# Kernel tuning notes

Hardware: AMD Instinct MI355X
Metric: run time of the kernel (lower is better)

The kernel has to match this reference:

```python
import jax, jax.numpy as jnp
import numpy as np

D = 512
H_G = 8
H_L = 8
WIN = 2
B = 4
S = 2048
LN_EPS = 1e-5


def layer_norm(x, g, b):
    m = jnp.mean(x, axis=-1, keepdims=True)
    v = jnp.mean(jnp.square(x - m), axis=-1, keepdims=True)
    return (x - m) * jax.lax.rsqrt(v + LN_EPS) * g + b


def mha(x, w_in, b_in, w_out, b_out, n_heads, mask=None):
    # x: [B', S', D]; w_in: [3D, D]; torch nn.MultiheadAttention math (eval, no dropout)
    Bp, Sp, Dm = x.shape
    dh = Dm // n_heads
    qkv = x @ w_in.T + b_in                      # [B', S', 3D]
    q, k, v = jnp.split(qkv, 3, axis=-1)
    sp = lambda t: t.reshape(Bp, Sp, n_heads, dh).transpose(0, 2, 1, 3)
    q, k, v = sp(q), sp(k), sp(v)                # [B', H, S', dh]
    scale = 1.0 / np.sqrt(dh).astype(np.float32)
    scores = jnp.einsum('bhqd,bhkd->bhqk', q, k) * scale
    if mask is not None:
        scores = scores + mask
    attn = jax.nn.softmax(scores, axis=-1)
    out = jnp.einsum('bhqk,bhkd->bhqd', attn, v)
    out = out.transpose(0, 2, 1, 3).reshape(Bp, Sp, Dm)
    return out @ w_out.T + b_out


def setup_inputs() -> dict:
    key = jax.random.key(0)
    ks = jax.random.split(key, 12)
    s = 0.02
    inp = {
        'x': jax.random.normal(ks[0], (B, S, D), jnp.float32),
        'ln1_g': jnp.ones((D,), jnp.float32), 'ln1_b': jnp.zeros((D,), jnp.float32),
        'ln2_g': jnp.ones((D,), jnp.float32), 'ln2_b': jnp.zeros((D,), jnp.float32),
        'ln3_g': jnp.ones((D,), jnp.float32), 'ln3_b': jnp.zeros((D,), jnp.float32),
        'gw_in': jax.random.normal(ks[1], (3 * D, D), jnp.float32) * s,
        'gb_in': jnp.zeros((3 * D,), jnp.float32),
        'gw_out': jax.random.normal(ks[2], (D, D), jnp.float32) * s,
        'gb_out': jnp.zeros((D,), jnp.float32),
        'lw_in': jax.random.normal(ks[3], (3 * D, D), jnp.float32) * s,
        'lb_in': jnp.zeros((3 * D,), jnp.float32),
        'lw_out': jax.random.normal(ks[4], (D, D), jnp.float32) * s,
        'lb_out': jnp.zeros((D,), jnp.float32),
        'gate_w': jax.random.normal(ks[5], (D, D), jnp.float32) * s,
        'gate_b': jnp.zeros((D,), jnp.float32),
        'ff_w1': jax.random.normal(ks[6], (4 * D, D), jnp.float32) * s,
        'ff_b1': jnp.zeros((4 * D,), jnp.float32),
        'ff_w2': jax.random.normal(ks[7], (D, 4 * D), jnp.float32) * s,
        'ff_b2': jnp.zeros((D,), jnp.float32),
    }
    return inp


def reference(x, ln1_g, ln1_b, ln2_g, ln2_b, ln3_g, ln3_b,
              gw_in, gb_in, gw_out, gb_out,
              lw_in, lb_in, lw_out, lb_out,
              gate_w, gate_b, ff_w1, ff_b1, ff_w2, ff_b2):
    Bb, Ss, Dm = x.shape
    x_norm = layer_norm(x, ln1_g, ln1_b)

    # global causal attention
    causal = jnp.triu(jnp.full((Ss, Ss), -jnp.inf, jnp.float32), 1)
    g_out = mha(x_norm, gw_in, gb_in, gw_out, gb_out, H_G, mask=causal)

    xl = x_norm.reshape(Bb * (Ss // WIN), WIN, Dm)
    l_out = mha(xl, lw_in, lb_in, lw_out, lb_out, H_L).reshape(Bb, Ss, Dm)

    gate = jax.nn.sigmoid(x_norm @ gate_w.T + gate_b)
    x = x + gate * g_out + (1.0 - gate) * l_out

    h = layer_norm(x, ln2_g, ln2_b)
    h = jax.nn.gelu(h @ ff_w1.T + ff_b1, approximate=False) @ ff_w2.T + ff_b2
    x = x + h
    return layer_norm(x, ln3_g, ln3_b)
```

## Files before the change

### kernel.cpp

```cpp
#include <hip/hip_runtime.h>
#include <math.h>
#include <stdint.h>

typedef unsigned short u16;
typedef __attribute__((ext_vector_type(4))) unsigned short u16x4;
typedef __attribute__((ext_vector_type(8))) unsigned short u16x8;
typedef __attribute__((ext_vector_type(8))) short s16x8;
typedef __attribute__((ext_vector_type(4))) float f32x4;

constexpr int Bc = 4;
constexpr int Sq = 2048;
constexpr int Dm = 512;
constexpr int Mrows = Bc * Sq;

__device__ inline float b2f(u16 h) {
  union { uint32_t u; float f; } x; x.u = (uint32_t)h << 16; return x.f;
}
__device__ inline u16 f2bf(float f) {
  union { float f; uint32_t u; } x; x.f = f;
  uint32_t r = (x.u + 0x7fffu + ((x.u >> 16) & 1u)) >> 16;
  return (u16)r;
}

constexpr size_t W_GWIN  = 0;
constexpr size_t W_LWIN  = 786432;
constexpr size_t W_GWOUT = 1572864;
constexpr size_t W_LWOUT = 1835008;
constexpr size_t W_GATE  = 2097152;
constexpr size_t W_FF1   = 2359296;
constexpr size_t W_FF2   = 3407872;
constexpr size_t W_TOTAL = 4456448;

__global__ __launch_bounds__(256) void wconv_kernel(
    const float* __restrict__ gw_in, const float* __restrict__ lw_in,
    const float* __restrict__ gw_out, const float* __restrict__ lw_out,
    const float* __restrict__ gate_w, const float* __restrict__ ff_w1,
    const float* __restrict__ ff_w2, u16* __restrict__ dst) {
  size_t idx = ((size_t)blockIdx.x * 256 + threadIdx.x) * 4;
  if (idx >= W_TOTAL) return;
  const float* src; size_t base;
  if      (idx < W_LWIN)  { src = gw_in;  base = W_GWIN;  }
  else if (idx < W_GWOUT) { src = lw_in;  base = W_LWIN;  }
  else if (idx < W_LWOUT) { src = gw_out; base = W_GWOUT; }
  else if (idx < W_GATE)  { src = lw_out; base = W_LWOUT; }
  else if (idx < W_FF1)   { src = gate_w; base = W_GATE;  }
  else if (idx < W_FF2)   { src = ff_w1;  base = W_FF1;   }
  else                    { src = ff_w2;  base = W_FF2;   }
  float4 v = *reinterpret_cast<const float4*>(src + (idx - base));
  u16x4 o = { f2bf(v.x), f2bf(v.y), f2bf(v.z), f2bf(v.w) };
  *reinterpret_cast<u16x4*>(dst + idx) = o;
}

template <bool OB>
__global__ __launch_bounds__(128) void ln_kernel(
    const float* __restrict__ in, const float* __restrict__ add,
    const float* __restrict__ g, const float* __restrict__ b,
    void* __restrict__ outp) {
  const int row = blockIdx.x;
  const int t = threadIdx.x;
  float4 v = reinterpret_cast<const float4*>(in + (size_t)row * Dm)[t];
  if (add != nullptr) {
    float4 a = reinterpret_cast<const float4*>(add + (size_t)row * Dm)[t];
    v.x += a.x; v.y += a.y; v.z += a.z; v.w += a.w;
  }
  float s  = v.x + v.y + v.z + v.w;
  float s2 = v.x*v.x + v.y*v.y + v.z*v.z + v.w*v.w;
  #pragma unroll
  for (int o = 32; o > 0; o >>= 1) {
    s  += __shfl_down(s, o);
    s2 += __shfl_down(s2, o);
  }
  __shared__ float rs[2], rs2[2];
  if ((t & 63) == 0) { rs[t >> 6] = s; rs2[t >> 6] = s2; }
  __syncthreads();
  const float mean = (rs[0] + rs[1]) * (1.0f / Dm);
  const float var  = (rs2[0] + rs2[1]) * (1.0f / Dm) - mean * mean;
  const float rstd = rsqrtf(var + 1e-5f);
  float4 gv = reinterpret_cast<const float4*>(g)[t];
  float4 bv = reinterpret_cast<const float4*>(b)[t];
  float ox = (v.x - mean) * rstd * gv.x + bv.x;
  float oy = (v.y - mean) * rstd * gv.y + bv.y;
  float oz = (v.z - mean) * rstd * gv.z + bv.z;
  float ow = (v.w - mean) * rstd * gv.w + bv.w;
  if (OB) {
    u16x4 o4 = { f2bf(ox), f2bf(oy), f2bf(oz), f2bf(ow) };
    *reinterpret_cast<u16x4*>((u16*)outp + (size_t)row * Dm + t * 4) = o4;
  } else {
    float4 o4; o4.x = ox; o4.y = oy; o4.z = oz; o4.w = ow;
    reinterpret_cast<float4*>((float*)outp + (size_t)row * Dm)[t] = o4;
  }
}

template <int ACT, bool OUT_BF16>
__global__ __launch_bounds__(256) void mfma_gemm(
    const u16* __restrict__ A, const u16* __restrict__ W,
    const float* __restrict__ bias, void* __restrict__ Cout, int N, int K) {
  __shared__ u16 sA[128 * 32];
  __shared__ u16 sW[128 * 32];
  const int tid  = threadIdx.x;
  const int wid  = tid >> 6, lane = tid & 63;
  const int lr   = lane & 15, kh = lane >> 4;
  const int wm   = wid >> 1, wn = wid & 1;
  const int m0   = blockIdx.y * 128, n0 = blockIdx.x * 128;
  const int row0 = tid >> 2,        ko0 = (tid & 3) * 8;
  const int row1 = (256 + tid) >> 2, ko1 = (tid & 3) * 8;

  f32x4 acc[4][4] = {};
  for (int k0 = 0; k0 < K; k0 += 32) {
    __syncthreads();
    __builtin_amdgcn_global_load_lds(
        (const __attribute__((address_space(1))) void*)(A + (size_t)(m0 + row0) * K + k0 + ko0),
        (__attribute__((address_space(3))) void*)(sA + wid * 512), 16, 0, 0);
    __builtin_amdgcn_global_load_lds(
        (const __attribute__((address_space(1))) void*)(A + (size_t)(m0 + row1) * K + k0 + ko1),
        (__attribute__((address_space(3))) void*)(sA + 2048 + wid * 512), 16, 0, 0);
    __builtin_amdgcn_global_load_lds(
        (const __attribute__((address_space(1))) void*)(W + (size_t)(n0 + row0) * K + k0 + ko0),
        (__attribute__((address_space(3))) void*)(sW + wid * 512), 16, 0, 0);
    __builtin_amdgcn_global_load_lds(
        (const __attribute__((address_space(1))) void*)(W + (size_t)(n0 + row1) * K + k0 + ko1),
        (__attribute__((address_space(3))) void*)(sW + 2048 + wid * 512), 16, 0, 0);
    __syncthreads();
    s16x8 af[4], bf[4];
    #pragma unroll
    for (int mf = 0; mf < 4; ++mf)
      af[mf] = *reinterpret_cast<const s16x8*>(&sA[(wm * 64 + mf * 16 + lr) * 32 + kh * 8]);
    #pragma unroll
    for (int nf = 0; nf < 4; ++nf)
      bf[nf] = *reinterpret_cast<const s16x8*>(&sW[(wn * 64 + nf * 16 + lr) * 32 + kh * 8]);
    #pragma unroll
    for (int mf = 0; mf < 4; ++mf)
      #pragma unroll
      for (int nf = 0; nf < 4; ++nf)
        acc[mf][nf] = __builtin_amdgcn_mfma_f32_16x16x32_bf16(af[mf], bf[nf], acc[mf][nf], 0, 0, 0);
  }
  #pragma unroll
  for (int nf = 0; nf < 4; ++nf) {
    const int col = n0 + wn * 64 + nf * 16 + lr;
    const float bv = bias[col];
    #pragma unroll
    for (int mf = 0; mf < 4; ++mf) {
      #pragma unroll
      for (int j = 0; j < 4; ++j) {
        const int rowg = m0 + wm * 64 + mf * 16 + kh * 4 + j;
        float v = acc[mf][nf][j] + bv;
        if (ACT == 1) v = 1.0f / (1.0f + expf(-v));
        else if (ACT == 2) v = 0.5f * v * (1.0f + erff(v * 0.70710678118654752440f));
        if (OUT_BF16) ((u16*)Cout)[(size_t)rowg * N + col] = f2bf(v);
        else          ((float*)Cout)[(size_t)rowg * N + col] = v;
      }
    }
  }
}

__global__ __launch_bounds__(256) void fuse3_kernel(
    const u16* __restrict__ A0, const u16* __restrict__ A1, const u16* __restrict__ A2,
    const u16* __restrict__ Wg, const u16* __restrict__ Wgo, const u16* __restrict__ Wlo,
    const float* __restrict__ bg, const float* __restrict__ bgo, const float* __restrict__ blo,
    const float* __restrict__ x, float* __restrict__ x2) {
  constexpr int N = 512, K = 512;
  __shared__ u16 sA[128 * 32];
  __shared__ u16 sW[128 * 32];
  const int tid  = threadIdx.x;
  const int wid  = tid >> 6, lane = tid & 63;
  const int lr   = lane & 15, kh = lane >> 4;
  const int wm   = wid >> 1, wn = wid & 1;
  const int m0   = blockIdx.y * 128, n0 = blockIdx.x * 128;
  const int row0 = tid >> 2,        ko0 = (tid & 3) * 8;
  const int row1 = (256 + tid) >> 2, ko1 = (tid & 3) * 8;

  f32x4 gv[4][4], pgv[4][4], acc[4][4];
  for (int pass = 0; pass < 3; ++pass) {
    const u16* A = (pass == 0) ? A0 : (pass == 1) ? A1 : A2;
    const u16* W = (pass == 0) ? Wg : (pass == 1) ? Wgo : Wlo;
    #pragma unroll
    for (int mf = 0; mf < 4; ++mf)
      #pragma unroll
      for (int nf = 0; nf < 4; ++nf)
        acc[mf][nf] = f32x4{0.f, 0.f, 0.f, 0.f};
    for (int k0 = 0; k0 < K; k0 += 32) {
      __syncthreads();
      __builtin_amdgcn_global_load_lds(
          (const __attribute__((address_space(1))) void*)(A + (size_t)(m0 + row0) * K + k0 + ko0),
          (__attribute__((address_space(3))) void*)(sA + wid * 512), 16, 0, 0);
      __builtin_amdgcn_global_load_lds(
          (const __attribute__((address_space(1))) void*)(A + (size_t)(m0 + row1) * K + k0 + ko1),
          (__attribute__((address_space(3))) void*)(sA + 2048 + wid * 512), 16, 0, 0);
      __builtin_amdgcn_global_load_lds(
          (const __attribute__((address_space(1))) void*)(W + (size_t)(n0 + row0) * K + k0 + ko0),
          (__attribute__((address_space(3))) void*)(sW + wid * 512), 16, 0, 0);
      __builtin_amdgcn_global_load_lds(
          (const __attribute__((address_space(1))) void*)(W + (size_t)(n0 + row1) * K + k0 + ko1),
          (__attribute__((address_space(3))) void*)(sW + 2048 + wid * 512), 16, 0, 0);
      __syncthreads();
      s16x8 af[4], bf[4];
      #pragma unroll
      for (int mf = 0; mf < 4; ++mf)
        af[mf] = *reinterpret_cast<const s16x8*>(&sA[(wm * 64 + mf * 16 + lr) * 32 + kh * 8]);
      #pragma unroll
      for (int nf = 0; nf < 4; ++nf)
        bf[nf] = *reinterpret_cast<const s16x8*>(&sW[(wn * 64 + nf * 16 + lr) * 32 + kh * 8]);
      #pragma unroll
      for (int mf = 0; mf < 4; ++mf)
        #pragma unroll
        for (int nf = 0; nf < 4; ++nf)
          acc[mf][nf] = __builtin_amdgcn_mfma_f32_16x16x32_bf16(af[mf], bf[nf], acc[mf][nf], 0, 0, 0);
    }
    if (pass == 0) {
      #pragma unroll
      for (int nf = 0; nf < 4; ++nf) {
        const float bv = bg[n0 + wn * 64 + nf * 16 + lr];
        #pragma unroll
        for (int mf = 0; mf < 4; ++mf)
          #pragma unroll
          for (int j = 0; j < 4; ++j)
            gv[mf][nf][j] = 1.0f / (1.0f + __expf(-(acc[mf][nf][j] + bv)));
      }
    } else if (pass == 1) {
      #pragma unroll
      for (int nf = 0; nf < 4; ++nf) {
        const float bv = bgo[n0 + wn * 64 + nf * 16 + lr];
        #pragma unroll
        for (int mf = 0; mf < 4; ++mf)
          #pragma unroll
          for (int j = 0; j < 4; ++j)
            pgv[mf][nf][j] = acc[mf][nf][j] + bv;
      }
    }
  }
  #pragma unroll
  for (int nf = 0; nf < 4; ++nf) {
    const int col = n0 + wn * 64 + nf * 16 + lr;
    const float bv = blo[col];
    #pragma unroll
    for (int mf = 0; mf < 4; ++mf) {
      #pragma unroll
      for (int j = 0; j < 4; ++j) {
        const int rowg = m0 + wm * 64 + mf * 16 + kh * 4 + j;
        const float pl = acc[mf][nf][j] + bv;
        const float g  = gv[mf][nf][j];
        const float pg = pgv[mf][nf][j];
        x2[(size_t)rowg * N + col] = x[(size_t)rowg * N + col] + g * pg + (1.0f - g) * pl;
      }
    }
  }
}

__global__ __launch_bounds__(256) void attn_global_kernel(
    const u16* __restrict__ qkv, u16* __restrict__ outb,
    float* __restrict__ opart, float* __restrict__ ml) {
  const int id = 79 - (int)blockIdx.x;
  int qt, s, ns;
  if (id < 8)       { qt = id;                s = 0;            ns = 1; }
  else if (id < 24) { int t = id - 8;  qt = 8 + (t >> 1);  s = t & 1;  ns = 2; }
  else if (id < 48) { int t = id - 24; int q3 = t / 3; qt = 16 + q3; s = t - q3 * 3; ns = 3; }
  else              { int t = id - 48; qt = 24 + (t >> 2); s = t & 3;  ns = 4; }
  const int kt0 = s * 8;
  const int kt1 = min(kt0 + 8, qt + 1);

  const int h  = blockIdx.y;
  const int b  = blockIdx.z;
  const int tid = threadIdx.x;
  const int w = tid >> 6, lane = tid & 63;
  const int c = lane & 15, kh = lane >> 4;

  __shared__ u16 Kb[64][72];
  __shared__ u16 Vt[64][72];
  __shared__ u16 Pw[4][16][72];

  const size_t bbase = (size_t)b * Sq;

  s16x8 aq[2];
  {
    const u16* qg = qkv + (bbase + qt * 64 + w * 16 + c) * 1536 + h * 64 + kh * 8;
    aq[0] = *reinterpret_cast<const s16x8*>(qg);
    aq[1] = *reinterpret_cast<const s16x8*>(qg + 32);
  }

  f32x4 o_acc[4] = {};
  float mrow[4] = { -INFINITY, -INFINITY, -INFINITY, -INFINITY };
  float lrow[4] = { 0.f, 0.f, 0.f, 0.f };
  int qp[4];
  #pragma unroll
  for (int j = 0; j < 4; ++j) qp[j] = qt * 64 + w * 16 + kh * 4 + j;

  const int g2 = tid >> 3, cc = tid & 7;
  const int srow2 = g2 * 2;
  const u16* kg0 = qkv + (bbase + srow2) * 1536 + 512 + h * 64 + cc * 8;
  const size_t tilestep = (size_t)64 * 1536;

  u16x8 ka, kb2, va, vb;
  {
    const u16* p = kg0 + (size_t)kt0 * tilestep;
    ka  = *reinterpret_cast<const u16x8*>(p);
    kb2 = *reinterpret_cast<const u16x8*>(p + 1536);
    va  = *reinterpret_cast<const u16x8*>(p + 512);
    vb  = *reinterpret_cast<const u16x8*>(p + 1536 + 512);
  }

  for (int kt = kt0; kt < kt1; ++kt) {
    __syncthreads();
    {
      *reinterpret_cast<u16x8*>(&Kb[srow2][cc * 8])     = ka;
      *reinterpret_cast<u16x8*>(&Kb[srow2 + 1][cc * 8]) = kb2;
      const int sw = srow2 ^ (cc * 8);
      #pragma unroll
      for (int i = 0; i < 8; ++i) {
        uint32_t pk = (uint32_t)va[i] | ((uint32_t)vb[i] << 16);
        *reinterpret_cast<uint32_t*>(&Vt[cc * 8 + i][sw]) = pk;
      }
    }
    __syncthreads();
    if (kt + 1 < kt1) {
      const u16* p = kg0 + (size_t)(kt + 1) * tilestep;
      ka  = *reinterpret_cast<const u16x8*>(p);
      kb2 = *reinterpret_cast<const u16x8*>(p + 1536);
      va  = *reinterpret_cast<const u16x8*>(p + 512);
      vb  = *reinterpret_cast<const u16x8*>(p + 1536 + 512);
    }

    f32x4 s_acc[4] = {};
    #pragma unroll
    for (int nb = 0; nb < 4; ++nb) {
      #pragma unroll
      for (int kk = 0; kk < 2; ++kk) {
        s16x8 bk = *reinterpret_cast<const s16x8*>(&Kb[nb * 16 + c][kk * 32 + kh * 8]);
        s_acc[nb] = __builtin_amdgcn_mfma_f32_16x16x32_bf16(aq[kk], bk, s_acc[nb], 0, 0, 0);
      }
    }

    const bool diag = (kt == qt);
    float p[4][4];
    float tm[4] = { -INFINITY, -INFINITY, -INFINITY, -INFINITY };
    #pragma unroll
    for (int nb = 0; nb < 4; ++nb) {
      #pragma unroll
      for (int j = 0; j < 4; ++j) {
        float sv = s_acc[nb][j] * 0.125f;
        if (diag && (kt * 64 + nb * 16 + c) > qp[j]) sv = -INFINITY;
        p[nb][j] = sv;
        tm[j] = fmaxf(tm[j], sv);
      }
    }
    #pragma unroll
    for (int o = 1; o < 16; o <<= 1) {
      #pragma unroll
      for (int j = 0; j < 4; ++j) tm[j] = fmaxf(tm[j], __shfl_xor(tm[j], o));
    }
    float corr[4], psum[4];
    #pragma unroll
    for (int j = 0; j < 4; ++j) {
      const float mnew = fmaxf(mrow[j], tm[j]);
      corr[j] = __expf(mrow[j] - mnew);
      mrow[j] = mnew;
      psum[j] = 0.f;
      #pragma unroll
      for (int nb = 0; nb < 4; ++nb) {
        p[nb][j] = __expf(p[nb][j] - mnew);
        psum[j] += p[nb][j];
      }
    }
    #pragma unroll
    for (int o = 1; o < 16; o <<= 1) {
      #pragma unroll
      for (int j = 0; j < 4; ++j) psum[j] += __shfl_xor(psum[j], o);
    }
    #pragma unroll
    for (int j = 0; j < 4; ++j) lrow[j] = lrow[j] * corr[j] + psum[j];
    #pragma unroll
    for (int nb2 = 0; nb2 < 4; ++nb2)
      #pragma unroll
      for (int j = 0; j < 4; ++j) o_acc[nb2][j] *= corr[j];

    #pragma unroll
    for (int nb = 0; nb < 4; ++nb)
      #pragma unroll
      for (int j = 0; j < 4; ++j)
        Pw[w][kh * 4 + j][nb * 16 + c] = f2bf(p[nb][j]);

    #pragma unroll
    for (int kk = 0; kk < 2; ++kk) {
      s16x8 ap = *reinterpret_cast<const s16x8*>(&Pw[w][c][kk * 32 + kh * 8]);
      #pragma unroll
      for (int nb2 = 0; nb2 < 4; ++nb2) {
        const int dh = nb2 * 16 + c;
        const int f8 = ((dh >> 3) & 7) * 8;
        s16x8 bv = *reinterpret_cast<const s16x8*>(&Vt[dh][(kk * 32 + kh * 8) ^ f8]);
        o_acc[nb2] = __builtin_amdgcn_mfma_f32_16x16x32_bf16(ap, bv, o_acc[nb2], 0, 0, 0);
      }
    }
  }

  if (ns == 1) {
    float invl[4];
    #pragma unroll
    for (int j = 0; j < 4; ++j) invl[j] = 1.0f / lrow[j];
    #pragma unroll
    for (int nb2 = 0; nb2 < 4; ++nb2)
      #pragma unroll
      for (int j = 0; j < 4; ++j) {
        const int qrow = qt * 64 + w * 16 + kh * 4 + j;
        outb[(bbase + qrow) * Dm + h * 64 + nb2 * 16 + c] = f2bf(o_acc[nb2][j] * invl[j]);
      }
  } else {
    const size_t pid = (size_t)(b * 8 + h) * 80 + id;
    float* op = opart + pid * 4096;
    #pragma unroll
    for (int nb2 = 0; nb2 < 4; ++nb2)
      #pragma unroll
      for (int j = 0; j < 4; ++j)
        op[(w * 16 + kh * 4 + j) * 64 + nb2 * 16 + c] = o_acc[nb2][j];
    if (c == 0) {
      #pragma unroll
      for (int j = 0; j < 4; ++j) {
        ml[pid * 128 + w * 16 + kh * 4 + j]      = mrow[j];
        ml[pid * 128 + 64 + w * 16 + kh * 4 + j] = lrow[j];
      }
    }
  }
}

__global__ __launch_bounds__(256) void attn_combine_kernel(
    const float* __restrict__ opart, const float* __restrict__ ml,
    u16* __restrict__ outb) {
  const int qt = 8 + (int)blockIdx.x;
  const int h = blockIdx.y, b = blockIdx.z;
  int ns, idb;
  if (qt < 16)      { ns = 2; idb = 8 + (qt - 8) * 2; }
  else if (qt < 24) { ns = 3; idb = 24 + (qt - 16) * 3; }
  else              { ns = 4; idb = 48 + (qt - 24) * 4; }
  const int r  = threadIdx.x >> 2;
  const int d0 = (threadIdx.x & 3) * 16;
  const size_t pidb = (size_t)(b * 8 + h) * 80 + idb;

  float M = -INFINITY;
  for (int s2 = 0; s2 < ns; ++s2)
    M = fmaxf(M, ml[(pidb + s2) * 128 + r]);
  float L = 0.f;
  f32x4 o0 = {}, o1 = {}, o2 = {}, o3 = {};
  for (int s2 = 0; s2 < ns; ++s2) {
    const size_t pp = pidb + s2;
    const float wgt = __expf(ml[pp * 128 + r] - M);
    L += wgt * ml[pp * 128 + 64 + r];
    const float* op = opart + pp * 4096 + (size_t)r * 64 + d0;
    f32x4 a0 = *reinterpret_cast<const f32x4*>(op);
    f32x4 a1 = *reinterpret_cast<const f32x4*>(op + 4);
    f32x4 a2 = *reinterpret_cast<const f32x4*>(op + 8);
    f32x4 a3 = *reinterpret_cast<const f32x4*>(op + 12);
    #pragma unroll
    for (int i = 0; i < 4; ++i) {
      o0[i] += wgt * a0[i]; o1[i] += wgt * a1[i];
      o2[i] += wgt * a2[i]; o3[i] += wgt * a3[i];
    }
  }
  const float invL = 1.0f / L;
  u16* dst = outb + ((size_t)b * Sq + qt * 64 + r) * Dm + h * 64 + d0;
  u16x4 w0 = { f2bf(o0[0]*invL), f2bf(o0[1]*invL), f2bf(o0[2]*invL), f2bf(o0[3]*invL) };
  u16x4 w1 = { f2bf(o1[0]*invL), f2bf(o1[1]*invL), f2bf(o1[2]*invL), f2bf(o1[3]*invL) };
  u16x4 w2 = { f2bf(o2[0]*invL), f2bf(o2[1]*invL), f2bf(o2[2]*invL), f2bf(o2[3]*invL) };
  u16x4 w3 = { f2bf(o3[0]*invL), f2bf(o3[1]*invL), f2bf(o3[2]*invL), f2bf(o3[3]*invL) };
  *reinterpret_cast<u16x4*>(dst)      = w0;
  *reinterpret_cast<u16x4*>(dst + 4)  = w1;
  *reinterpret_cast<u16x4*>(dst + 8)  = w2;
  *reinterpret_cast<u16x4*>(dst + 12) = w3;
}

__global__ __launch_bounds__(256) void attn_local_kernel(
    const u16* __restrict__ qkv, u16* __restrict__ outb) {
  const int unit = blockIdx.x * 4 + (threadIdx.x >> 6);
  const int lane = threadIdx.x & 63;
  const int h = unit & 7;
  const size_t pair = (size_t)(unit >> 3);
  const u16* r0 = qkv + pair * 2 * 1536;
  const u16* r1 = r0 + 1536;
  const int off = h * 64 + lane;
  const float q0 = b2f(r0[off]), k0 = b2f(r0[512 + off]), v0 = b2f(r0[1024 + off]);
  const float q1 = b2f(r1[off]), k1 = b2f(r1[512 + off]), v1 = b2f(r1[1024 + off]);
  float s00 = q0 * k0, s01 = q0 * k1, s10 = q1 * k0, s11 = q1 * k1;
  #pragma unroll
  for (int o = 1; o < 64; o <<= 1) {
    s00 += __shfl_xor(s00, o); s01 += __shfl_xor(s01, o);
    s10 += __shfl_xor(s10, o); s11 += __shfl_xor(s11, o);
  }
  s00 *= 0.125f; s01 *= 0.125f; s10 *= 0.125f; s11 *= 0.125f;
  const float m0 = fmaxf(s00, s01), m1 = fmaxf(s10, s11);
  const float e00 = expf(s00 - m0), e01 = expf(s01 - m0);
  const float e10 = expf(s10 - m1), e11 = expf(s11 - m1);
  const float w0 = 1.0f / (e00 + e01), w1 = 1.0f / (e10 + e11);
  outb[pair * 2 * Dm + off]       = f2bf((e00 * v0 + e01 * v1) * w0);
  outb[(pair * 2 + 1) * Dm + off] = f2bf((e10 * v0 + e11 * v1) * w1);
}

extern "C" void kernel_launch(void* const* d_in, const int* in_sizes, int n_in,
                              void* d_out, int out_size, void* d_ws, size_t ws_size,
                              hipStream_t stream) {
  const float* x      = (const float*)d_in[0];
  const float* ln1_g  = (const float*)d_in[1];
  const float* ln1_b  = (const float*)d_in[2];
  const float* ln2_g  = (const float*)d_in[3];
  const float* ln2_b  = (const float*)d_in[4];
  const float* ln3_g  = (const float*)d_in[5];
  const float* ln3_b  = (const float*)d_in[6];
  const float* gw_in  = (const float*)d_in[7];
  const float* gb_in  = (const float*)d_in[8];
  const float* gw_out = (const float*)d_in[9];
  const float* gb_out = (const float*)d_in[10];
  const float* lw_in  = (const float*)d_in[11];
  const float* lb_in  = (const float*)d_in[12];
  const float* lw_out = (const float*)d_in[13];
  const float* lb_out = (const float*)d_in[14];
  const float* gate_w = (const float*)d_in[15];
  const float* gate_b = (const float*)d_in[16];
  const float* ff_w1  = (const float*)d_in[17];
  const float* ff_b1  = (const float*)d_in[18];
  const float* ff_w2  = (const float*)d_in[19];
  const float* ff_b2  = (const float*)d_in[20];
  float* out = (float*)d_out;
  char* wsb  = (char*)d_ws;

  float* opart = (float*)(wsb + 0);
  float* ml    = (float*)(wsb + 41943040);
  float* x2    = (float*)(wsb + 0);
  float* h2    = (float*)(wsb + 16777216);
  u16*   xnb   = (u16*)(wsb + 67108864);
  u16*   qkvb  = (u16*)(wsb + 75497472);
  u16*   attgb = (u16*)(wsb + 100663296);
  u16*   attlb = (u16*)(wsb + 109051904);
  u16*   wb    = (u16*)(wsb + 117440512);
  u16*   ff1b  = qkvb;

  wconv_kernel<<<(W_TOTAL / 4 + 255) / 256, 256, 0, stream>>>(
      gw_in, lw_in, gw_out, lw_out, gate_w, ff_w1, ff_w2, wb);
  ln_kernel<true><<<Mrows, 128, 0, stream>>>(x, nullptr, ln1_g, ln1_b, xnb);
  mfma_gemm<0, true><<<dim3(1536 / 128, Mrows / 128), 256, 0, stream>>>(
      xnb, wb + W_LWIN, lb_in, qkvb, 1536, 512);
  attn_local_kernel<<<(Mrows / 2) * 8 / 4, 256, 0, stream>>>(qkvb, attlb);
  mfma_gemm<0, true><<<dim3(1536 / 128, Mrows / 128), 256, 0, stream>>>(
      xnb, wb + W_GWIN, gb_in, qkvb, 1536, 512);
  attn_global_kernel<<<dim3(80, 8, Bc), 256, 0, stream>>>(qkvb, attgb, opart, ml);
  attn_combine_kernel<<<dim3(24, 8, Bc), 256, 0, stream>>>(opart, ml, attgb);
  fuse3_kernel<<<dim3(512 / 128, Mrows / 128), 256, 0, stream>>>(
      xnb, attgb, attlb, wb + W_GATE, wb + W_GWOUT, wb + W_LWOUT,
      gate_b, gb_out, lb_out, x, x2);
  ln_kernel<true><<<Mrows, 128, 0, stream>>>(x2, nullptr, ln2_g, ln2_b, xnb);
  mfma_gemm<2, true><<<dim3(2048 / 128, Mrows / 128), 256, 0, stream>>>(
      xnb, wb + W_FF1, ff_b1, ff1b, 2048, 512);
  mfma_gemm<0, false><<<dim3(512 / 128, Mrows / 128), 256, 0, stream>>>(
      ff1b, wb + W_FF2, ff_b2, h2, 512, 2048);
  ln_kernel<false><<<Mrows, 128, 0, stream>>>(x2, h2, ln3_g, ln3_b, out);
}
```

Measured before the change: 298.4 us.

## Merge QKV GEMMs, split-K the FF2 GEMM, use exp2 softmax in attention

The global and local QKV projections become a single GEMM of width 3072, which relies on the global and local in_proj weights sitting next to each other in the bf16 weight buffer; a second bias pointer is selected by column. The FF2 GEMM (K=2048, only 256 tiles) is split-K into two halves that write separate fp32 buffers, and the final layernorm sums both. Global attention now works in the exp2 domain with a prescaled log2e factor and defers the row-sum shuffle reduction to after the key loop, and the partial buffer indexing is compacted to 72 slots. The aim is fewer launches, better GPU occupancy for the FF2 GEMM, and less per-tile shuffle work, at the cost of an extra fp32 partial buffer read and write.

```diff
diff --git a/kernel.cpp b/kernel.cpp
--- a/kernel.cpp
+++ b/kernel.cpp
@@ -12,6 +12,7 @@
 constexpr int Sq = 2048;
 constexpr int Dm = 512;
 constexpr int Mrows = Bc * Sq;
+constexpr int QW = 3072;
 
 __device__ inline float b2f(u16 h) {
   union { uint32_t u; float f; } x; x.u = (uint32_t)h << 16; return x.f;
@@ -54,6 +55,7 @@
 template <bool OB>
 __global__ __launch_bounds__(128) void ln_kernel(
     const float* __restrict__ in, const float* __restrict__ add,
+    const float* __restrict__ add2,
     const float* __restrict__ g, const float* __restrict__ b,
     void* __restrict__ outp) {
   const int row = blockIdx.x;
@@ -61,6 +63,10 @@
   float4 v = reinterpret_cast<const float4*>(in + (size_t)row * Dm)[t];
   if (add != nullptr) {
     float4 a = reinterpret_cast<const float4*>(add + (size_t)row * Dm)[t];
+    v.x += a.x; v.y += a.y; v.z += a.z; v.w += a.w;
+  }
+  if (add2 != nullptr) {
+    float4 a = reinterpret_cast<const float4*>(add2 + (size_t)row * Dm)[t];
     v.x += a.x; v.y += a.y; v.z += a.z; v.w += a.w;
   }
   float s  = v.x + v.y + v.z + v.w;
@@ -94,7 +100,8 @@
 template <int ACT, bool OUT_BF16>
 __global__ __launch_bounds__(256) void mfma_gemm(
     const u16* __restrict__ A, const u16* __restrict__ W,
-    const float* __restrict__ bias, void* __restrict__ Cout, int N, int K) {
+    const float* __restrict__ bias, const float* __restrict__ bias2, int bsplit,
+    void* __restrict__ Cout, int N, int K) {
   __shared__ u16 sA[128 * 32];
   __shared__ u16 sW[128 * 32];
   const int tid  = threadIdx.x;
@@ -137,7 +144,7 @@
   #pragma unroll
   for (int nf = 0; nf < 4; ++nf) {
     const int col = n0 + wn * 64 + nf * 16 + lr;
-    const float bv = bias[col];
+    const float bv = (bias2 != nullptr && col >= bsplit) ? bias2[col - bsplit] : bias[col];
     #pragma unroll
     for (int mf = 0; mf < 4; ++mf) {
       #pragma unroll
@@ -148,6 +155,67 @@
         else if (ACT == 2) v = 0.5f * v * (1.0f + erff(v * 0.70710678118654752440f));
         if (OUT_BF16) ((u16*)Cout)[(size_t)rowg * N + col] = f2bf(v);
         else          ((float*)Cout)[(size_t)rowg * N + col] = v;
+      }
+    }
+  }
+}
+
+__global__ __launch_bounds__(256) void mfma_gemm_sk(
+    const u16* __restrict__ A, const u16* __restrict__ W,
+    const float* __restrict__ bias, float* __restrict__ C0, float* __restrict__ C1,
+    int N, int Kt) {
+  __shared__ u16 sA[128 * 32];
+  __shared__ u16 sW[128 * 32];
+  const int tid  = threadIdx.x;
+  const int wid  = tid >> 6, lane = tid & 63;
+  const int lr   = lane & 15, kh = lane >> 4;
+  const int wm   = wid >> 1, wn = wid & 1;
+  const int m0   = blockIdx.y * 128, n0 = blockIdx.x * 128;
+  const int z    = blockIdx.z;
+  const int kbeg = z * (Kt / 2), kend = kbeg + (Kt / 2);
+  const int row0 = tid >> 2,        ko0 = (tid & 3) * 8;
+  const int row1 = (256 + tid) >> 2, ko1 = (tid & 3) * 8;
+
+  f32x4 acc[4][4] = {};
+  for (int k0 = kbeg; k0 < kend; k0 += 32) {
+    __syncthreads();
+    __builtin_amdgcn_global_load_lds(
+        (const __attribute__((address_space(1))) void*)(A + (size_t)(m0 + row0) * Kt + k0 + ko0),
+        (__attribute__((address_space(3))) void*)(sA + wid * 512), 16, 0, 0);
+    __builtin_amdgcn_global_load_lds(
+        (const __attribute__((address_space(1))) void*)(A + (size_t)(m0 + row1) * Kt + k0 + ko1),
+        (__attribute__((address_space(3))) void*)(sA + 2048 + wid * 512), 16, 0, 0);
+    __builtin_amdgcn_global_load_lds(
+        (const __attribute__((address_space(1))) void*)(W + (size_t)(n0 + row0) * Kt + k0 + ko0),
+        (__attribute__((address_space(3))) void*)(sW + wid * 512), 16, 0, 0);
+    __builtin_amdgcn_global_load_lds(
+        (const __attribute__((address_space(1))) void*)(W + (size_t)(n0 + row1) * Kt + k0 + ko1),
+        (__attribute__((address_space(3))) void*)(sW + 2048 + wid * 512), 16, 0, 0);
+    __syncthreads();
+    s16x8 af[4], bf[4];
+    #pragma unroll
+    for (int mf = 0; mf < 4; ++mf)
+      af[mf] = *reinterpret_cast<const s16x8*>(&sA[(wm * 64 + mf * 16 + lr) * 32 + kh * 8]);
+    #pragma unroll
+    for (int nf = 0; nf < 4; ++nf)
+      bf[nf] = *reinterpret_cast<const s16x8*>(&sW[(wn * 64 + nf * 16 + lr) * 32 + kh * 8]);
+    #pragma unroll
+    for (int mf = 0; mf < 4; ++mf)
+      #pragma unroll
+      for (int nf = 0; nf < 4; ++nf)
+        acc[mf][nf] = __builtin_amdgcn_mfma_f32_16x16x32_bf16(af[mf], bf[nf], acc[mf][nf], 0, 0, 0);
+  }
+  float* C = z ? C1 : C0;
+  #pragma unroll
+  for (int nf = 0; nf < 4; ++nf) {
+    const int col = n0 + wn * 64 + nf * 16 + lr;
+    const float bv = z ? 0.0f : bias[col];
+    #pragma unroll
+    for (int mf = 0; mf < 4; ++mf) {
+      #pragma unroll
+      for (int j = 0; j < 4; ++j) {
+        const int rowg = m0 + wm * 64 + mf * 16 + kh * 4 + j;
+        C[(size_t)rowg * N + col] = acc[mf][nf][j] + bv;
       }
     }
   }
@@ -263,6 +331,7 @@
   const int tid = threadIdx.x;
   const int w = tid >> 6, lane = tid & 63;
   const int c = lane & 15, kh = lane >> 4;
+  constexpr float TS = 0.125f * 1.44269504088896f;
 
   __shared__ u16 Kb[64][72];
   __shared__ u16 Vt[64][72];
@@ -272,7 +341,7 @@
 
   s16x8 aq[2];
   {
-    const u16* qg = qkv + (bbase + qt * 64 + w * 16 + c) * 1536 + h * 64 + kh * 8;
+    const u16* qg = qkv + (bbase + qt * 64 + w * 16 + c) * QW + h * 64 + kh * 8;
     aq[0] = *reinterpret_cast<const s16x8*>(qg);
     aq[1] = *reinterpret_cast<const s16x8*>(qg + 32);
   }
@@ -286,16 +355,16 @@
 
   const int g2 = tid >> 3, cc = tid & 7;
   const int srow2 = g2 * 2;
-  const u16* kg0 = qkv + (bbase + srow2) * 1536 + 512 + h * 64 + cc * 8;
-  const size_t tilestep = (size_t)64 * 1536;
+  const u16* kg0 = qkv + (bbase + srow2) * QW + 512 + h * 64 + cc * 8;
+  const size_t tilestep = (size_t)64 * QW;
 
   u16x8 ka, kb2, va, vb;
   {
     const u16* p = kg0 + (size_t)kt0 * tilestep;
     ka  = *reinterpret_cast<const u16x8*>(p);
-    kb2 = *reinterpret_cast<const u16x8*>(p + 1536);
+    kb2 = *reinterpret_cast<const u16x8*>(p + QW);
     va  = *reinterpret_cast<const u16x8*>(p + 512);
-    vb  = *reinterpret_cast<const u16x8*>(p + 1536 + 512);
+    vb  = *reinterpret_cast<const u16x8*>(p + QW + 512);
   }
 
   for (int kt = kt0; kt < kt1; ++kt) {
@@ -314,9 +383,9 @@
     if (kt + 1 < kt1) {
       const u16* p = kg0 + (size_t)(kt + 1) * tilestep;
       ka  = *reinterpret_cast<const u16x8*>(p);
-      kb2 = *reinterpret_cast<const u16x8*>(p + 1536);
+      kb2 = *reinterpret_cast<const u16x8*>(p + QW);
       va  = *reinterpret_cast<const u16x8*>(p + 512);
-      vb  = *reinterpret_cast<const u16x8*>(p + 1536 + 512);
+      vb  = *reinterpret_cast<const u16x8*>(p + QW + 512);
     }
 
     f32x4 s_acc[4] = {};
@@ -336,7 +405,7 @@
     for (int nb = 0; nb < 4; ++nb) {
       #pragma unroll
       for (int j = 0; j < 4; ++j) {
-        float sv = s_acc[nb][j] * 0.125f;
+        float sv = s_acc[nb][j] * TS;
         if (diag && (kt * 64 + nb * 16 + c) > qp[j]) sv = -INFINITY;
         p[nb][j] = sv;
         tm[j] = fmaxf(tm[j], sv);
@@ -347,30 +416,21 @@
       #pragma unroll
       for (int j = 0; j < 4; ++j) tm[j] = fmaxf(tm[j], __shfl_xor(tm[j], o));
     }
-    float corr[4], psum[4];
     #pragma unroll
     for (int j = 0; j < 4; ++j) {
       const float mnew = fmaxf(mrow[j], tm[j]);
-      corr[j] = __expf(mrow[j] - mnew);
+      const float corr = exp2f(mrow[j] - mnew);
       mrow[j] = mnew;
-      psum[j] = 0.f;
+      float ps = 0.f;
       #pragma unroll
       for (int nb = 0; nb < 4; ++nb) {
-        p[nb][j] = __expf(p[nb][j] - mnew);
-        psum[j] += p[nb][j];
-      }
-    }
-    #pragma unroll
-    for (int o = 1; o < 16; o <<= 1) {
-      #pragma unroll
-      for (int j = 0; j < 4; ++j) psum[j] += __shfl_xor(psum[j], o);
-    }
-    #pragma unroll
-    for (int j = 0; j < 4; ++j) lrow[j] = lrow[j] * corr[j] + psum[j];
-    #pragma unroll
-    for (int nb2 = 0; nb2 < 4; ++nb2)
-      #pragma unroll
-      for (int j = 0; j < 4; ++j) o_acc[nb2][j] *= corr[j];
+        p[nb][j] = exp2f(p[nb][j] - mnew);
+        ps += p[nb][j];
+      }
+      lrow[j] = lrow[j] * corr + ps;
+      #pragma unroll
+      for (int nb2 = 0; nb2 < 4; ++nb2) o_acc[nb2][j] *= corr;
+    }
 
     #pragma unroll
     for (int nb = 0; nb < 4; ++nb)
@@ -391,6 +451,12 @@
     }
   }
 
+  #pragma unroll
+  for (int o = 1; o < 16; o <<= 1) {
+    #pragma unroll
+    for (int j = 0; j < 4; ++j) lrow[j] += __shfl_xor(lrow[j], o);
+  }
+
   if (ns == 1) {
     float invl[4];
     #pragma unroll
@@ -403,7 +469,7 @@
         outb[(bbase + qrow) * Dm + h * 64 + nb2 * 16 + c] = f2bf(o_acc[nb2][j] * invl[j]);
       }
   } else {
-    const size_t pid = (size_t)(b * 8 + h) * 80 + id;
+    const size_t pid = (size_t)(b * 8 + h) * 72 + (id - 8);
     float* op = opart + pid * 4096;
     #pragma unroll
     for (int nb2 = 0; nb2 < 4; ++nb2)
@@ -426,12 +492,12 @@
   const int qt = 8 + (int)blockIdx.x;
   const int h = blockIdx.y, b = blockIdx.z;
   int ns, idb;
-  if (qt < 16)      { ns = 2; idb = 8 + (qt - 8) * 2; }
-  else if (qt < 24) { ns = 3; idb = 24 + (qt - 16) * 3; }
-  else              { ns = 4; idb = 48 + (qt - 24) * 4; }
+  if (qt < 16)      { ns = 2; idb = (qt - 8) * 2; }
+  else if (qt < 24) { ns = 3; idb = 16 + (qt - 16) * 3; }
+  else              { ns = 4; idb = 40 + (qt - 24) * 4; }
   const int r  = threadIdx.x >> 2;
   const int d0 = (threadIdx.x & 3) * 16;
-  const size_t pidb = (size_t)(b * 8 + h) * 80 + idb;
+  const size_t pidb = (size_t)(b * 8 + h) * 72 + idb;
 
   float M = -INFINITY;
   for (int s2 = 0; s2 < ns; ++s2)
@@ -440,7 +506,7 @@
   f32x4 o0 = {}, o1 = {}, o2 = {}, o3 = {};
   for (int s2 = 0; s2 < ns; ++s2) {
     const size_t pp = pidb + s2;
-    const float wgt = __expf(ml[pp * 128 + r] - M);
+    const float wgt = exp2f(ml[pp * 128 + r] - M);
     L += wgt * ml[pp * 128 + 64 + r];
     const float* op = opart + pp * 4096 + (size_t)r * 64 + d0;
     f32x4 a0 = *reinterpret_cast<const f32x4*>(op);
@@ -471,8 +537,8 @@
   const int lane = threadIdx.x & 63;
   const int h = unit & 7;
   const size_t pair = (size_t)(unit >> 3);
-  const u16* r0 = qkv + pair * 2 * 1536;
-  const u16* r1 = r0 + 1536;
+  const u16* r0 = qkv + pair * 2 * QW + 1536;
+  const u16* r1 = r0 + QW;
   const int off = h * 64 + lane;
   const float q0 = b2f(r0[off]), k0 = b2f(r0[512 + off]), v0 = b2f(r0[1024 + off]);
   const float q1 = b2f(r1[off]), k1 = b2f(r1[512 + off]), v1 = b2f(r1[1024 + off]);
@@ -518,34 +584,33 @@
   float* out = (float*)d_out;
   char* wsb  = (char*)d_ws;
 
-  float* opart = (float*)(wsb + 0);
-  float* ml    = (float*)(wsb + 41943040);
-  float* x2    = (float*)(wsb + 0);
-  float* h2    = (float*)(wsb + 16777216);
-  u16*   xnb   = (u16*)(wsb + 67108864);
-  u16*   qkvb  = (u16*)(wsb + 75497472);
-  u16*   attgb = (u16*)(wsb + 100663296);
-  u16*   attlb = (u16*)(wsb + 109051904);
-  u16*   wb    = (u16*)(wsb + 117440512);
+  u16*   xnb   = (u16*)(wsb + 0);
+  u16*   qkvb  = (u16*)(wsb + 8388608);
   u16*   ff1b  = qkvb;
+  float* h2b   = (float*)(wsb + 41943040);
+  u16*   attgb = (u16*)(wsb + 58720256);
+  u16*   attlb = (u16*)(wsb + 67108864);
+  u16*   wb    = (u16*)(wsb + 75497472);
+  float* opart = (float*)(wsb + 84410368);
+  float* ml    = (float*)(wsb + 122159104);
+  float* x2    = (float*)(wsb + 84410368);
+  float* h2a   = (float*)(wsb + 101187584);
 
   wconv_kernel<<<(W_TOTAL / 4 + 255) / 256, 256, 0, stream>>>(
       gw_in, lw_in, gw_out, lw_out, gate_w, ff_w1, ff_w2, wb);
-  ln_kernel<true><<<Mrows, 128, 0, stream>>>(x, nullptr, ln1_g, ln1_b, xnb);
-  mfma_gemm<0, true><<<dim3(1536 / 128, Mrows / 128), 256, 0, stream>>>(
-      xnb, wb + W_LWIN, lb_in, qkvb, 1536, 512);
+  ln_kernel<true><<<Mrows, 128, 0, stream>>>(x, nullptr, nullptr, ln1_g, ln1_b, xnb);
+  mfma_gemm<0, true><<<dim3(QW / 128, Mrows / 128), 256, 0, stream>>>(
+      xnb, wb, gb_in, lb_in, 1536, qkvb, QW, 512);
   attn_local_kernel<<<(Mrows / 2) * 8 / 4, 256, 0, stream>>>(qkvb, attlb);
-  mfma_gemm<0, true><<<dim3(1536 / 128, Mrows / 128), 256, 0, stream>>>(
-      xnb, wb + W_GWIN, gb_in, qkvb, 1536, 512);
   attn_global_kernel<<<dim3(80, 8, Bc), 256, 0, stream>>>(qkvb, attgb, opart, ml);
   attn_combine_kernel<<<dim3(24, 8, Bc), 256, 0, stream>>>(opart, ml, attgb);
   fuse3_kernel<<<dim3(512 / 128, Mrows / 128), 256, 0, stream>>>(
       xnb, attgb, attlb, wb + W_GATE, wb + W_GWOUT, wb + W_LWOUT,
       gate_b, gb_out, lb_out, x, x2);
-  ln_kernel<true><<<Mrows, 128, 0, stream>>>(x2, nullptr, ln2_g, ln2_b, xnb);
+  ln_kernel<true><<<Mrows, 128, 0, stream>>>(x2, nullptr, nullptr, ln2_g, ln2_b, xnb);
   mfma_gemm<2, true><<<dim3(2048 / 128, Mrows / 128), 256, 0, stream>>>(
-      xnb, wb + W_FF1, ff_b1, ff1b, 2048, 512);
-  mfma_gemm<0, false><<<dim3(512 / 128, Mrows / 128), 256, 0, stream>>>(
-      ff1b, wb + W_FF2, ff_b2, h2, 512, 2048);
-  ln_kernel<false><<<Mrows, 128, 0, stream>>>(x2, h2, ln3_g, ln3_b, out);
-}
+      xnb, wb + W_FF1, ff_b1, nullptr, 0, ff1b, 2048, 512);
+  mfma_gemm_sk<<<dim3(512 / 128, Mrows / 128, 2), 256, 0, stream>>>(
+      ff1b, wb + W_FF2, ff_b2, h2a, h2b, 512, 2048);
+  ln_kernel<false><<<Mrows, 128, 0, stream>>>(x2, h2a, h2b, ln3_g, ln3_b, out);
+}
```

After: 280.2 us. -6.1%, faster.
